# Optimization experiments

Hardware: AMD Instinct MI355X
Metric: run time of the kernel (lower is better)

The kernel has to match this reference:

```python
import jax, jax.numpy as jnp
import numpy as np

N_NODES = 50000
N_EDGES = 625000
D_IN, D_HID, D_OUT = 512, 128, 1


def gcn_conv(x, W, b, src, dst, n_nodes):
    """PyG GCNConv: add self-loops, symmetric D^-1/2 (A+I) D^-1/2 normalization.
    x: [N, d_in], W: [d_in, d_out], b: [d_out], src/dst: [E] int.
    """
    xw = x @ W  # [N, d_out] - linear before propagation (PyG order)
    # degree including self-loop
    deg = jax.ops.segment_sum(jnp.ones_like(src, dtype=xw.dtype), dst,
                              num_segments=n_nodes) + 1.0
    dinv = jax.lax.rsqrt(deg)  # [N]
    norm = dinv[src] * dinv[dst]  # [E]
    # neighbor aggregation (scatter-add over destination nodes)
    agg = jax.ops.segment_sum(xw[src] * norm[:, None], dst, num_segments=n_nodes)
    # self-loop contribution: norm_ii = dinv_i^2
    agg = agg + xw * (dinv * dinv)[:, None]
    return agg + b


def layer_norm(x, gamma, beta, eps=1e-5):
    mu = jnp.mean(x, axis=-1, keepdims=True)
    var = jnp.var(x, axis=-1, keepdims=True)
    return (x - mu) * jax.lax.rsqrt(var + eps) * gamma + beta


def setup_inputs() -> dict:
    key = jax.random.key(0)
    ks = jax.random.split(key, 12)
    x = jax.random.normal(ks[0], (N_NODES, D_IN), dtype=jnp.float32)
    edge_index = jax.random.randint(ks[1], (2, N_EDGES), 0, N_NODES, dtype=jnp.int64)

    def glorot(k, shape):
        lim = np.sqrt(6.0 / (shape[0] + shape[1]))
        return jax.random.uniform(k, shape, jnp.float32, -lim, lim)

    return {
        "x": x,
        "W1": glorot(ks[2], (D_IN, D_HID)), "b1": jnp.zeros((D_HID,), jnp.float32),
        "gamma1": jnp.ones((D_HID,), jnp.float32), "beta1": jnp.zeros((D_HID,), jnp.float32),
        "W2": glorot(ks[3], (D_HID, D_HID)), "b2": jnp.zeros((D_HID,), jnp.float32),
        "W3": glorot(ks[4], (D_HID, D_HID)), "b3": jnp.zeros((D_HID,), jnp.float32),
        "W4": glorot(ks[5], (D_HID, D_OUT)), "b4": jnp.zeros((D_OUT,), jnp.float32),
        "edge_index": edge_index,
    }


def reference(x, W1, b1, gamma1, beta1, W2, b2, W3, b3, W4, b4, edge_index):
    # eval mode: F.dropout(training=False) is identity
    src, dst = edge_index[0], edge_index[1]
    n = x.shape[0]
    h = jax.nn.relu(layer_norm(gcn_conv(x, W1, b1, src, dst, n), gamma1, beta1))
    h = jax.nn.relu(gcn_conv(h, W2, b2, src, dst, n))
    h = jax.nn.relu(gcn_conv(h, W3, b3, src, dst, n))
    h = gcn_conv(h, W4, b4, src, dst, n)
    return jnp.squeeze(h, axis=-1)  # [N]
```

## Files before the change

### kernel.cpp

```cpp
#include <hip/hip_runtime.h>
#include <hip/hip_bf16.h>
#include <cstdint>

#define D_IN 512
#define D_HID 128

typedef unsigned short u16;
typedef unsigned int u32;
typedef __attribute__((ext_vector_type(8))) short short8;
typedef __attribute__((ext_vector_type(4))) float f32x4;

__device__ __forceinline__ u16 f2bf(float f) {
    u32 u = __float_as_uint(f);
    u = (u + 0x7FFFu + ((u >> 16) & 1u)) >> 16;
    return (u16)u;
}
__device__ __forceinline__ float bfc(short x) {
    return __uint_as_float(((u32)(u16)x) << 16);
}

__global__ __launch_bounds__(256) void k_deg_int(const int* __restrict__ dst,
                                                 int* __restrict__ deg, int E) {
    int e = blockIdx.x * 256 + threadIdx.x;
    if (e < E) atomicAdd(&deg[dst[e]], 1);
}

__global__ __launch_bounds__(256) void k_scan_block(const int* __restrict__ deg,
                                                    int* __restrict__ rowptr,
                                                    int* __restrict__ bsum, int N) {
    __shared__ int sh[256];
    int i = blockIdx.x * 256 + threadIdx.x;
    int v = (i < N) ? deg[i] : 0;
    sh[threadIdx.x] = v;
    __syncthreads();
#pragma unroll
    for (int off = 1; off < 256; off <<= 1) {
        int t = (threadIdx.x >= off) ? sh[threadIdx.x - off] : 0;
        __syncthreads();
        sh[threadIdx.x] += t;
        __syncthreads();
    }
    int incl = sh[threadIdx.x];
    if (i < N) rowptr[i] = incl - v;
    if (threadIdx.x == 255) bsum[blockIdx.x] = incl;
}

__global__ __launch_bounds__(256) void k_scan_partials(int* __restrict__ bsum, int P) {
    __shared__ int sh[256];
    int v = (threadIdx.x < P) ? bsum[threadIdx.x] : 0;
    sh[threadIdx.x] = v;
    __syncthreads();
#pragma unroll
    for (int off = 1; off < 256; off <<= 1) {
        int t = (threadIdx.x >= off) ? sh[threadIdx.x - off] : 0;
        __syncthreads();
        sh[threadIdx.x] += t;
        __syncthreads();
    }
    if (threadIdx.x < P) bsum[threadIdx.x] = sh[threadIdx.x] - v;
}

__global__ __launch_bounds__(256) void k_apply_offset(int* __restrict__ rowptr,
                                                      const int* __restrict__ bsum,
                                                      int* __restrict__ deg_cursor,
                                                      float* __restrict__ dinv,
                                                      int N, int E) {
    int i = blockIdx.x * 256 + threadIdx.x;
    if (i == 0) rowptr[N] = E;
    if (i >= N) return;
    int dv = deg_cursor[i];
    int rp = rowptr[i] + bsum[i >> 8];
    rowptr[i] = rp;
    deg_cursor[i] = rp;
    dinv[i] = rsqrtf((float)dv + 1.0f);
}

__global__ __launch_bounds__(256) void k_fill_csr(const int* __restrict__ src,
                                                  const int* __restrict__ dst,
                                                  int* __restrict__ cursor,
                                                  int* __restrict__ csr, int E) {
    int e = blockIdx.x * 256 + threadIdx.x;
    if (e >= E) return;
    int pos = atomicAdd(&cursor[dst[e]], 1);
    csr[pos] = src[e];
}

__global__ __launch_bounds__(256) void k_wt_all(const float* __restrict__ W1,
                                                const float* __restrict__ W2,
                                                const float* __restrict__ W3,
                                                u16* __restrict__ WT1,
                                                u16* __restrict__ WT2,
                                                u16* __restrict__ WT3) {
    int t = blockIdx.x * 256 + threadIdx.x;
    if (t < 65536) {
        int c = t >> 9, k = t & 511;
        WT1[t] = f2bf(W1[(size_t)k * 128 + c]);
    } else if (t < 65536 + 16384) {
        int u = t - 65536;
        int c = u >> 7, k = u & 127;
        WT2[u] = f2bf(W2[(size_t)k * 128 + c]);
    } else if (t < 65536 + 32768) {
        int u = t - 65536 - 16384;
        int c = u >> 7, k = u & 127;
        WT3[u] = f2bf(W3[(size_t)k * 128 + c]);
    }
}

template <int K, typename TI>
__global__ __launch_bounds__(256) void k_gemm_mfma(const TI* __restrict__ X,
                                                   const u16* __restrict__ WT,
                                                   u16* __restrict__ Y, int N) {
    __shared__ u16 Xs[64 * 40];
    __shared__ u16 Ws[128 * 40];
    const int tid = threadIdx.x;
    const int wv = tid >> 6;
    const int lane = tid & 63;
    const int row0 = blockIdx.x * 64;
    const int rsel = lane & 15;
    const int kgrp = (lane >> 4) * 8;

    f32x4 acc[8];
#pragma unroll
    for (int c = 0; c < 8; ++c) acc[c] = (f32x4){0.f, 0.f, 0.f, 0.f};

    for (int k0 = 0; k0 < K; k0 += 32) {
        {
            int r = tid >> 2;
            int kk = (tid & 3) * 8;
            int row = row0 + r;
            if constexpr (sizeof(TI) == 4) {
                float v[8];
                if (row < N) {
                    float4 p0 = *(const float4*)&X[(size_t)row * K + k0 + kk];
                    float4 p1 = *(const float4*)&X[(size_t)row * K + k0 + kk + 4];
                    v[0] = p0.x; v[1] = p0.y; v[2] = p0.z; v[3] = p0.w;
                    v[4] = p1.x; v[5] = p1.y; v[6] = p1.z; v[7] = p1.w;
                } else {
#pragma unroll
                    for (int i = 0; i < 8; ++i) v[i] = 0.f;
                }
                union { u16 us[8]; short8 v8; } tmp;
#pragma unroll
                for (int i = 0; i < 8; ++i) tmp.us[i] = f2bf(v[i]);
                *(short8*)&Xs[r * 40 + kk] = tmp.v8;
            } else {
                short8 v8 = {};
                if (row < N) v8 = *(const short8*)&X[(size_t)row * K + k0 + kk];
                *(short8*)&Xs[r * 40 + kk] = v8;
            }
        }
        {
            int col = tid >> 1;
            int kh = (tid & 1) * 16;
            const u16* g = &WT[(size_t)col * K + k0 + kh];
            u16* d = &Ws[col * 40 + kh];
            *(short8*)d = *(const short8*)g;
            *(short8*)(d + 8) = *(const short8*)(g + 8);
        }
        __syncthreads();
        short8 a = *(const short8*)&Xs[(wv * 16 + rsel) * 40 + kgrp];
#pragma unroll
        for (int c = 0; c < 8; ++c) {
            short8 b = *(const short8*)&Ws[(c * 16 + rsel) * 40 + kgrp];
            acc[c] = __builtin_amdgcn_mfma_f32_16x16x32_bf16(a, b, acc[c], 0, 0, 0);
        }
        __syncthreads();
    }
#pragma unroll
    for (int r = 0; r < 4; ++r) {
        int row = row0 + wv * 16 + (lane >> 4) * 4 + r;
        if (row < N) {
#pragma unroll
            for (int c = 0; c < 8; ++c)
                Y[(size_t)row * 128 + c * 16 + rsel] = f2bf(acc[c][r]);
        }
    }
}

#define GATHER_CORE(XW, rowptr, csr, dinv, node, q, es, a)                         \
    int beg = rowptr[node], end = rowptr[node + 1];                                \
    float a[8];                                                                    \
    _Pragma("unroll") for (int i = 0; i < 8; ++i) a[i] = 0.f;                      \
    {                                                                              \
        int j = beg + es;                                                          \
        for (; j + 4 < end; j += 8) {                                              \
            int s0 = csr[j], s1 = csr[j + 4];                                      \
            float w0 = dinv[s0], w1 = dinv[s1];                                    \
            short8 r0 = *(const short8*)&XW[(size_t)s0 * 128 + q * 8];             \
            short8 r1 = *(const short8*)&XW[(size_t)s1 * 128 + q * 8];             \
            _Pragma("unroll") for (int i = 0; i < 8; ++i)                          \
                a[i] += bfc(r0[i]) * w0 + bfc(r1[i]) * w1;                         \
        }                                                                          \
        if (j < end) {                                                             \
            int s = csr[j];                                                        \
            float w = dinv[s];                                                     \
            short8 r = *(const short8*)&XW[(size_t)s * 128 + q * 8];               \
            _Pragma("unroll") for (int i = 0; i < 8; ++i) a[i] += bfc(r[i]) * w;   \
        }                                                                          \
    }                                                                              \
    _Pragma("unroll") for (int i = 0; i < 8; ++i) {                                \
        a[i] += __shfl_xor(a[i], 16);                                              \
        a[i] += __shfl_xor(a[i], 32);                                              \
    }

__global__ __launch_bounds__(256) void k_gather_ln_relu(const u16* __restrict__ XW,
                                                        const int* __restrict__ rowptr,
                                                        const int* __restrict__ csr,
                                                        const float* __restrict__ dinv,
                                                        const float* __restrict__ b,
                                                        const float* __restrict__ gamma,
                                                        const float* __restrict__ beta,
                                                        u16* __restrict__ H, int N) {
    int node = blockIdx.x * 4 + (threadIdx.x >> 6);
    int lane = threadIdx.x & 63;
    int q = lane & 15;
    int es = lane >> 4;
    if (node >= N) return;
    float di = dinv[node];
    GATHER_CORE(XW, rowptr, csr, dinv, node, q, es, a)
    short8 us = *(const short8*)&XW[(size_t)node * 128 + q * 8];
    float d2 = di * di;
    float4 b0 = *(const float4*)&b[q * 8];
    float4 b1 = *(const float4*)&b[q * 8 + 4];
    float v[8];
#pragma unroll
    for (int i = 0; i < 8; ++i) {
        float bb = (i < 4) ? ((const float*)&b0)[i] : ((const float*)&b1)[i - 4];
        v[i] = a[i] * di + bfc(us[i]) * d2 + bb;
    }
    float s = 0.f, sq = 0.f;
#pragma unroll
    for (int i = 0; i < 8; ++i) { s += v[i]; sq += v[i] * v[i]; }
#pragma unroll
    for (int off = 8; off; off >>= 1) {
        s  += __shfl_xor(s, off);
        sq += __shfl_xor(sq, off);
    }
    float mu  = s * (1.f / 128.f);
    float var = sq * (1.f / 128.f) - mu * mu;
    float rr  = rsqrtf(var + 1e-5f);
    float4 g0 = *(const float4*)&gamma[q * 8];
    float4 g1 = *(const float4*)&gamma[q * 8 + 4];
    float4 e0 = *(const float4*)&beta[q * 8];
    float4 e1 = *(const float4*)&beta[q * 8 + 4];
    if (es == 0) {
        union { u16 us[8]; short8 v8; } o;
#pragma unroll
        for (int i = 0; i < 8; ++i) {
            float gg = (i < 4) ? ((const float*)&g0)[i] : ((const float*)&g1)[i - 4];
            float ee = (i < 4) ? ((const float*)&e0)[i] : ((const float*)&e1)[i - 4];
            o.us[i] = f2bf(fmaxf((v[i] - mu) * rr * gg + ee, 0.f));
        }
        *(short8*)&H[(size_t)node * 128 + q * 8] = o.v8;
    }
}

__global__ __launch_bounds__(256) void k_gather_relu(const u16* __restrict__ XW,
                                                     const int* __restrict__ rowptr,
                                                     const int* __restrict__ csr,
                                                     const float* __restrict__ dinv,
                                                     const float* __restrict__ b,
                                                     u16* __restrict__ H, int N) {
    int node = blockIdx.x * 4 + (threadIdx.x >> 6);
    int lane = threadIdx.x & 63;
    int q = lane & 15;
    int es = lane >> 4;
    if (node >= N) return;
    float di = dinv[node];
    GATHER_CORE(XW, rowptr, csr, dinv, node, q, es, a)
    if (es != 0) return;
    short8 us = *(const short8*)&XW[(size_t)node * 128 + q * 8];
    float d2 = di * di;
    float4 b0 = *(const float4*)&b[q * 8];
    float4 b1 = *(const float4*)&b[q * 8 + 4];
    union { u16 us[8]; short8 v8; } o;
#pragma unroll
    for (int i = 0; i < 8; ++i) {
        float bb = (i < 4) ? ((const float*)&b0)[i] : ((const float*)&b1)[i - 4];
        o.us[i] = f2bf(fmaxf(a[i] * di + bfc(us[i]) * d2 + bb, 0.f));
    }
    *(short8*)&H[(size_t)node * 128 + q * 8] = o.v8;
}

__global__ __launch_bounds__(256) void k_gather_dot(const u16* __restrict__ XW,
                                                    const int* __restrict__ rowptr,
                                                    const int* __restrict__ csr,
                                                    const float* __restrict__ dinv,
                                                    const float* __restrict__ b,
                                                    const float* __restrict__ W4,
                                                    float* __restrict__ XW4, int N) {
    int node = blockIdx.x * 4 + (threadIdx.x >> 6);
    int lane = threadIdx.x & 63;
    int q = lane & 15;
    int es = lane >> 4;
    if (node >= N) return;
    float di = dinv[node];
    GATHER_CORE(XW, rowptr, csr, dinv, node, q, es, a)
    short8 us = *(const short8*)&XW[(size_t)node * 128 + q * 8];
    float d2 = di * di;
    float4 b0 = *(const float4*)&b[q * 8];
    float4 b1 = *(const float4*)&b[q * 8 + 4];
    float4 w0 = *(const float4*)&W4[q * 8];
    float4 w1 = *(const float4*)&W4[q * 8 + 4];
    float t = 0.f;
#pragma unroll
    for (int i = 0; i < 8; ++i) {
        float bb = (i < 4) ? ((const float*)&b0)[i] : ((const float*)&b1)[i - 4];
        float ww = (i < 4) ? ((const float*)&w0)[i] : ((const float*)&w1)[i - 4];
        float v = fmaxf(a[i] * di + bfc(us[i]) * d2 + bb, 0.f);
        t += v * ww;
    }
#pragma unroll
    for (int off = 8; off; off >>= 1) t += __shfl_xor(t, off);
    if (lane == 0) XW4[node] = t;
}

__global__ __launch_bounds__(256) void k_final_scalar(const float* __restrict__ XW4,
                                                      const int* __restrict__ rowptr,
                                                      const int* __restrict__ csr,
                                                      const float* __restrict__ dinv,
                                                      const float* __restrict__ b4,
                                                      float* __restrict__ OUT, int N) {
    int node = blockIdx.x * 16 + (threadIdx.x >> 4);
    int q = threadIdx.x & 15;
    if (node >= N) return;
    int beg = rowptr[node], end = rowptr[node + 1];
    float acc = 0.f;
    for (int j = beg + q; j < end; j += 16) {
        int s = csr[j];
        acc += XW4[s] * dinv[s];
    }
#pragma unroll
    for (int off = 8; off; off >>= 1) acc += __shfl_xor(acc, off);
    if (q == 0) {
        float di = dinv[node];
        OUT[node] = acc * di + XW4[node] * di * di + b4[0];
    }
}

static inline size_t alignup(size_t x) { return (x + 255) & ~(size_t)255; }

extern "C" void kernel_launch(void* const* d_in, const int* in_sizes, int n_in,
                              void* d_out, int out_size, void* d_ws, size_t ws_size,
                              hipStream_t stream) {
    const float* x      = (const float*)d_in[0];
    const float* W1     = (const float*)d_in[1];
    const float* b1     = (const float*)d_in[2];
    const float* gamma1 = (const float*)d_in[3];
    const float* beta1  = (const float*)d_in[4];
    const float* W2     = (const float*)d_in[5];
    const float* b2     = (const float*)d_in[6];
    const float* W3     = (const float*)d_in[7];
    const float* b3     = (const float*)d_in[8];
    const float* W4     = (const float*)d_in[9];
    const float* b4     = (const float*)d_in[10];
    const int*   ei     = (const int*)d_in[11];

    const int N = in_sizes[0] / D_IN;
    const int E = in_sizes[11] / 2;
    const int* src = ei;
    const int* dst = ei + E;

    char* ws = (char*)d_ws;
    size_t off = 0;
    int*   deg_cur = (int*)(ws + off);   off += alignup((size_t)N * 4);
    int*   rowptr  = (int*)(ws + off);   off += alignup((size_t)(N + 1) * 4);
    int*   bsum    = (int*)(ws + off);   off += alignup(256 * 4);
    float* dinv    = (float*)(ws + off); off += alignup((size_t)N * 4);
    float* xw4     = (float*)(ws + off); off += alignup((size_t)N * 4);
    int*   csr     = (int*)(ws + off);   off += alignup((size_t)E * 4);
    u16*   WT1     = (u16*)(ws + off);   off += alignup((size_t)128 * 512 * 2);
    u16*   WT2     = (u16*)(ws + off);   off += alignup((size_t)128 * 128 * 2);
    u16*   WT3     = (u16*)(ws + off);   off += alignup((size_t)128 * 128 * 2);
    u16*   XW      = (u16*)(ws + off);   off += alignup((size_t)N * 128 * 2);
    u16*   H       = (u16*)(ws + off);

    const int scanBlocks = (N + 255) / 256;

    hipMemsetAsync(deg_cur, 0, (size_t)N * 4, stream);
    k_deg_int<<<(E + 255) / 256, 256, 0, stream>>>(dst, deg_cur, E);
    k_scan_block<<<scanBlocks, 256, 0, stream>>>(deg_cur, rowptr, bsum, N);
    k_scan_partials<<<1, 256, 0, stream>>>(bsum, scanBlocks);
    k_apply_offset<<<scanBlocks, 256, 0, stream>>>(rowptr, bsum, deg_cur, dinv, N, E);
    k_fill_csr<<<(E + 255) / 256, 256, 0, stream>>>(src, dst, deg_cur, csr, E);

    k_wt_all<<<(65536 + 32768 + 255) / 256, 256, 0, stream>>>(W1, W2, W3, WT1, WT2, WT3);

    const int gemmGrid   = (N + 63) / 64;
    const int gatherGrid = (N + 3) / 4;

    k_gemm_mfma<512, float><<<gemmGrid, 256, 0, stream>>>(x, WT1, XW, N);
    k_gather_ln_relu<<<gatherGrid, 256, 0, stream>>>(XW, rowptr, csr, dinv,
                                                     b1, gamma1, beta1, H, N);
    k_gemm_mfma<128, u16><<<gemmGrid, 256, 0, stream>>>(H, WT2, XW, N);
    k_gather_relu<<<gatherGrid, 256, 0, stream>>>(XW, rowptr, csr, dinv, b2, H, N);
    k_gemm_mfma<128, u16><<<gemmGrid, 256, 0, stream>>>(H, WT3, XW, N);
    k_gather_dot<<<gatherGrid, 256, 0, stream>>>(XW, rowptr, csr, dinv, b3, W4, xw4, N);
    k_final_scalar<<<(N + 15) / 16, 256, 0, stream>>>(xw4, rowptr, csr, dinv,
                                                      b4, (float*)d_out, N);
}
```

Before: 375.4 us.

## Prescale GEMM outputs by dinv to drop per-edge dinv gathers; fuse scan kernels

Each GEMM epilogue now multiplies its output row by dinv of the source node. The gather kernels then sum plain neighbor rows and scale once by the destination's dinv, which removes a random dinv load and a multiply per edge. The gather loop is also unrolled to four neighbors per iteration for more memory-level parallelism. The partial-scan kernel is folded into apply_offset, where each block redundantly rescans the block sums, saving one launch. The pre-scaled values are rounded to bf16 after scaling, which shifts numerics slightly.

```diff
diff --git a/kernel.cpp b/kernel.cpp
--- a/kernel.cpp
+++ b/kernel.cpp
@@ -45,7 +45,11 @@
     if (threadIdx.x == 255) bsum[blockIdx.x] = incl;
 }
 
-__global__ __launch_bounds__(256) void k_scan_partials(int* __restrict__ bsum, int P) {
+__global__ __launch_bounds__(256) void k_apply_offset(int* __restrict__ rowptr,
+                                                      const int* __restrict__ bsum,
+                                                      int* __restrict__ deg_cursor,
+                                                      float* __restrict__ dinv,
+                                                      int N, int E, int P) {
     __shared__ int sh[256];
     int v = (threadIdx.x < P) ? bsum[threadIdx.x] : 0;
     sh[threadIdx.x] = v;
@@ -57,19 +61,12 @@
         sh[threadIdx.x] += t;
         __syncthreads();
     }
-    if (threadIdx.x < P) bsum[threadIdx.x] = sh[threadIdx.x] - v;
-}
-
-__global__ __launch_bounds__(256) void k_apply_offset(int* __restrict__ rowptr,
-                                                      const int* __restrict__ bsum,
-                                                      int* __restrict__ deg_cursor,
-                                                      float* __restrict__ dinv,
-                                                      int N, int E) {
+    int boff = (blockIdx.x == 0) ? 0 : sh[blockIdx.x - 1];
     int i = blockIdx.x * 256 + threadIdx.x;
     if (i == 0) rowptr[N] = E;
     if (i >= N) return;
     int dv = deg_cursor[i];
-    int rp = rowptr[i] + bsum[i >> 8];
+    int rp = rowptr[i] + boff;
     rowptr[i] = rp;
     deg_cursor[i] = rp;
     dinv[i] = rsqrtf((float)dv + 1.0f);
@@ -109,6 +106,7 @@
 template <int K, typename TI>
 __global__ __launch_bounds__(256) void k_gemm_mfma(const TI* __restrict__ X,
                                                    const u16* __restrict__ WT,
+                                                   const float* __restrict__ dinv,
                                                    u16* __restrict__ Y, int N) {
     __shared__ u16 Xs[64 * 40];
     __shared__ u16 Ws[128 * 40];
@@ -170,32 +168,41 @@
     for (int r = 0; r < 4; ++r) {
         int row = row0 + wv * 16 + (lane >> 4) * 4 + r;
         if (row < N) {
+            float ds = dinv[row];
 #pragma unroll
             for (int c = 0; c < 8; ++c)
-                Y[(size_t)row * 128 + c * 16 + rsel] = f2bf(acc[c][r]);
+                Y[(size_t)row * 128 + c * 16 + rsel] = f2bf(acc[c][r] * ds);
         }
     }
 }
 
-#define GATHER_CORE(XW, rowptr, csr, dinv, node, q, es, a)                         \
+#define GATHER_CORE(XW, rowptr, csr, node, q, es, a)                               \
     int beg = rowptr[node], end = rowptr[node + 1];                                \
     float a[8];                                                                    \
     _Pragma("unroll") for (int i = 0; i < 8; ++i) a[i] = 0.f;                      \
     {                                                                              \
         int j = beg + es;                                                          \
-        for (; j + 4 < end; j += 8) {                                              \
+        for (; j + 12 < end; j += 16) {                                            \
+            int s0 = csr[j], s1 = csr[j + 4], s2 = csr[j + 8], s3 = csr[j + 12];   \
+            short8 r0 = *(const short8*)&XW[(size_t)s0 * 128 + q * 8];             \
+            short8 r1 = *(const short8*)&XW[(size_t)s1 * 128 + q * 8];             \
+            short8 r2 = *(const short8*)&XW[(size_t)s2 * 128 + q * 8];             \
+            short8 r3 = *(const short8*)&XW[(size_t)s3 * 128 + q * 8];             \
+            _Pragma("unroll") for (int i = 0; i < 8; ++i)                          \
+                a[i] += (bfc(r0[i]) + bfc(r1[i])) + (bfc(r2[i]) + bfc(r3[i]));     \
+        }                                                                          \
+        if (j + 4 < end) {                                                         \
             int s0 = csr[j], s1 = csr[j + 4];                                      \
-            float w0 = dinv[s0], w1 = dinv[s1];                                    \
             short8 r0 = *(const short8*)&XW[(size_t)s0 * 128 + q * 8];             \
             short8 r1 = *(const short8*)&XW[(size_t)s1 * 128 + q * 8];             \
             _Pragma("unroll") for (int i = 0; i < 8; ++i)                          \
-                a[i] += bfc(r0[i]) * w0 + bfc(r1[i]) * w1;                         \
+                a[i] += bfc(r0[i]) + bfc(r1[i]);                                   \
+            j += 8;                                                                \
         }                                                                          \
         if (j < end) {                                                             \
             int s = csr[j];                                                        \
-            float w = dinv[s];                                                     \
             short8 r = *(const short8*)&XW[(size_t)s * 128 + q * 8];               \
-            _Pragma("unroll") for (int i = 0; i < 8; ++i) a[i] += bfc(r[i]) * w;   \
+            _Pragma("unroll") for (int i = 0; i < 8; ++i) a[i] += bfc(r[i]);       \
         }                                                                          \
     }                                                                              \
     _Pragma("unroll") for (int i = 0; i < 8; ++i) {                                \
@@ -217,16 +224,15 @@
     int es = lane >> 4;
     if (node >= N) return;
     float di = dinv[node];
-    GATHER_CORE(XW, rowptr, csr, dinv, node, q, es, a)
+    GATHER_CORE(XW, rowptr, csr, node, q, es, a)
     short8 us = *(const short8*)&XW[(size_t)node * 128 + q * 8];
-    float d2 = di * di;
     float4 b0 = *(const float4*)&b[q * 8];
     float4 b1 = *(const float4*)&b[q * 8 + 4];
     float v[8];
 #pragma unroll
     for (int i = 0; i < 8; ++i) {
         float bb = (i < 4) ? ((const float*)&b0)[i] : ((const float*)&b1)[i - 4];
-        v[i] = a[i] * di + bfc(us[i]) * d2 + bb;
+        v[i] = (a[i] + bfc(us[i])) * di + bb;
     }
     float s = 0.f, sq = 0.f;
 #pragma unroll
@@ -267,17 +273,16 @@
     int es = lane >> 4;
     if (node >= N) return;
     float di = dinv[node];
-    GATHER_CORE(XW, rowptr, csr, dinv, node, q, es, a)
+    GATHER_CORE(XW, rowptr, csr, node, q, es, a)
     if (es != 0) return;
     short8 us = *(const short8*)&XW[(size_t)node * 128 + q * 8];
-    float d2 = di * di;
     float4 b0 = *(const float4*)&b[q * 8];
     float4 b1 = *(const float4*)&b[q * 8 + 4];
     union { u16 us[8]; short8 v8; } o;
 #pragma unroll
     for (int i = 0; i < 8; ++i) {
         float bb = (i < 4) ? ((const float*)&b0)[i] : ((const float*)&b1)[i - 4];
-        o.us[i] = f2bf(fmaxf(a[i] * di + bfc(us[i]) * d2 + bb, 0.f));
+        o.us[i] = f2bf(fmaxf((a[i] + bfc(us[i])) * di + bb, 0.f));
     }
     *(short8*)&H[(size_t)node * 128 + q * 8] = o.v8;
 }
@@ -295,9 +300,8 @@
     int es = lane >> 4;
     if (node >= N) return;
     float di = dinv[node];
-    GATHER_CORE(XW, rowptr, csr, dinv, node, q, es, a)
+    GATHER_CORE(XW, rowptr, csr, node, q, es, a)
     short8 us = *(const short8*)&XW[(size_t)node * 128 + q * 8];
-    float d2 = di * di;
     float4 b0 = *(const float4*)&b[q * 8];
     float4 b1 = *(const float4*)&b[q * 8 + 4];
     float4 w0 = *(const float4*)&W4[q * 8];
@@ -307,12 +311,12 @@
     for (int i = 0; i < 8; ++i) {
         float bb = (i < 4) ? ((const float*)&b0)[i] : ((const float*)&b1)[i - 4];
         float ww = (i < 4) ? ((const float*)&w0)[i] : ((const float*)&w1)[i - 4];
-        float v = fmaxf(a[i] * di + bfc(us[i]) * d2 + bb, 0.f);
+        float v = fmaxf((a[i] + bfc(us[i])) * di + bb, 0.f);
         t += v * ww;
     }
 #pragma unroll
     for (int off = 8; off; off >>= 1) t += __shfl_xor(t, off);
-    if (lane == 0) XW4[node] = t;
+    if (lane == 0) XW4[node] = t * di;
 }
 
 __global__ __launch_bounds__(256) void k_final_scalar(const float* __restrict__ XW4,
@@ -327,14 +331,12 @@
     int beg = rowptr[node], end = rowptr[node + 1];
     float acc = 0.f;
     for (int j = beg + q; j < end; j += 16) {
-        int s = csr[j];
-        acc += XW4[s] * dinv[s];
+        acc += XW4[csr[j]];
     }
 #pragma unroll
     for (int off = 8; off; off >>= 1) acc += __shfl_xor(acc, off);
     if (q == 0) {
-        float di = dinv[node];
-        OUT[node] = acc * di + XW4[node] * di * di + b4[0];
+        OUT[node] = dinv[node] * (acc + XW4[node]) + b4[0];
     }
 }
 
@@ -380,8 +382,8 @@
     hipMemsetAsync(deg_cur, 0, (size_t)N * 4, stream);
     k_deg_int<<<(E + 255) / 256, 256, 0, stream>>>(dst, deg_cur, E);
     k_scan_block<<<scanBlocks, 256, 0, stream>>>(deg_cur, rowptr, bsum, N);
-    k_scan_partials<<<1, 256, 0, stream>>>(bsum, scanBlocks);
-    k_apply_offset<<<scanBlocks, 256, 0, stream>>>(rowptr, bsum, deg_cur, dinv, N, E);
+    k_apply_offset<<<scanBlocks, 256, 0, stream>>>(rowptr, bsum, deg_cur, dinv,
+                                                   N, E, scanBlocks);
     k_fill_csr<<<(E + 255) / 256, 256, 0, stream>>>(src, dst, deg_cur, csr, E);
 
     k_wt_all<<<(65536 + 32768 + 255) / 256, 256, 0, stream>>>(W1, W2, W3, WT1, WT2, WT3);
@@ -389,12 +391,12 @@
     const int gemmGrid   = (N + 63) / 64;
     const int gatherGrid = (N + 3) / 4;
 
-    k_gemm_mfma<512, float><<<gemmGrid, 256, 0, stream>>>(x, WT1, XW, N);
+    k_gemm_mfma<512, float><<<gemmGrid, 256, 0, stream>>>(x, WT1, dinv, XW, N);
     k_gather_ln_relu<<<gatherGrid, 256, 0, stream>>>(XW, rowptr, csr, dinv,
                                                      b1, gamma1, beta1, H, N);
-    k_gemm_mfma<128, u16><<<gemmGrid, 256, 0, stream>>>(H, WT2, XW, N);
+    k_gemm_mfma<128, u16><<<gemmGrid, 256, 0, stream>>>(H, WT2, dinv, XW, N);
     k_gather_relu<<<gatherGrid, 256, 0, stream>>>(XW, rowptr, csr, dinv, b2, H, N);
-    k_gemm_mfma<128, u16><<<gemmGrid, 256, 0, stream>>>(H, WT3, XW, N);
+    k_gemm_mfma<128, u16><<<gemmGrid, 256, 0, stream>>>(H, WT3, dinv, XW, N);
     k_gather_dot<<<gatherGrid, 256, 0, stream>>>(XW, rowptr, csr, dinv, b3, W4, xw4, N);
     k_final_scalar<<<(N + 15) / 16, 256, 0, stream>>>(xw4, rowptr, csr, dinv,
                                                       b4, (float*)d_out, N);
```

Result: no change. 374.2 us (-0.3%).
